# Performance work log

Measured on AMD Instinct MI355X. Metric: run time of the kernel, lower is better.

The kernel has to match this reference:

```python
import jax, jax.numpy as jnp
import numpy as np
import math

BLOCK = 8
N_COEFF = BLOCK * BLOCK  # 64
N_SAMPLE = 250
SEED = 0  # args.seed

# zigzag order: flat index m*8+n from the hardcoded loc table
ZIGZAG = jnp.array([
    0, 1, 8, 16, 9, 2, 3, 10, 17, 24, 32, 25, 18, 11, 4, 5,
    12, 19, 26, 33, 40, 48, 41, 34, 27, 20, 13, 6, 7, 14, 21, 28,
    35, 42, 49, 56, 57, 50, 43, 36, 29, 22, 15, 23, 30, 37, 44, 51,
    58, 59, 52, 45, 38, 31, 39, 46, 53, 60, 61, 54, 47, 55, 62, 63
], dtype=jnp.int32)


def dct_matrix():
    Q = np.zeros((BLOCK, BLOCK), dtype=np.float32)
    Q[0, :] = math.sqrt(1.0 / BLOCK)
    for i in range(1, BLOCK):
        for j in range(BLOCK):
            Q[i, j] = math.sqrt(2.0 / BLOCK) * math.cos((2 * j + 1) * math.pi * i / (2.0 * BLOCK))
    return jnp.asarray(Q)


def setup_inputs() -> dict:
    key = jax.random.key(0)
    x = jax.random.uniform(key, (64, 3, 512, 512), dtype=jnp.float32)
    return {"x": x}


def reference(x):
    Q = dct_matrix()
    # rgb -> ycbcr, luminance channel only (module discards Cb/Cr)
    x255 = x * 255.0
    y = (0.299 * x255[:, 0] + 0.587 * x255[:, 1] + 0.114 * x255[:, 2]) / 255.0  # [B,H,W]
    B, H, W = y.shape
    a, b = H // BLOCK, W // BLOCK
    # split into 8x8 blocks: [B, a, b, 8, 8]
    blocks = y.reshape(B, a, BLOCK, b, BLOCK).transpose(0, 1, 3, 2, 4)
    # per-block 2D DCT: Q @ block @ Q^T, batched as one einsum
    dct = jnp.einsum('ij,nabjk,lk->nabil', Q, blocks, Q)  # [B,a,b,8,8]
    image_dct_result = dct.transpose(0, 1, 3, 2, 4).reshape(B, 1, H, W)
    # zigzag gather over flattened block coefficients -> [B, 64, a*b]
    dist = dct.reshape(B, a * b, N_COEFF)[:, :, ZIGZAG].transpose(0, 2, 1)
    # per (sample, coefficient) random permutation sampling of 250 blocks
    keys = jax.random.split(jax.random.key(SEED), B * N_COEFF)
    idx = jax.vmap(lambda k: jax.random.permutation(k, a * b)[:N_SAMPLE])(keys)
    idx = idx.reshape(B, N_COEFF, N_SAMPLE)
    dct_coeff_sample = jnp.take_along_axis(dist, idx, axis=2)  # [B,64,250]
    return image_dct_result, dct_coeff_sample
```

## Files before the change

kernel.cpp:

```cpp
#include <hip/hip_runtime.h>
#include <hip/hip_bf16.h>
#include <cstdint>


#define BATCH 64
#define HW 512
#define NBLK 4096
#define NSAMPLE 250
#define IMG_ELEMS (HW * HW)

#define A0 0.35355339059327373f
#define A1 0.49039264020161522f
#define A2 0.46193976625564337f
#define A3 0.41573480615127262f
#define A4 0.35355339059327379f
#define A5 0.27778511650980111f
#define A6 0.19134171618254492f
#define A7 0.09754516100806412f

__constant__ float Qc[8][8] = {
    { A0,  A0,  A0,  A0,  A0,  A0,  A0,  A0},
    { A1,  A3,  A5,  A7, -A7, -A5, -A3, -A1},
    { A2,  A6, -A6, -A2, -A2, -A6,  A6,  A2},
    { A3, -A7, -A1, -A5,  A5,  A1,  A7, -A3},
    { A4, -A4, -A4,  A4,  A4, -A4, -A4,  A4},
    { A5, -A1,  A7,  A3, -A3, -A7,  A1, -A5},
    { A6, -A2,  A2, -A6, -A6,  A2, -A2,  A6},
    { A7, -A5,  A3, -A1,  A1, -A3,  A5, -A7},
};

__constant__ int ZIGZAG[64] = {
    0, 1, 8, 16, 9, 2, 3, 10, 17, 24, 32, 25, 18, 11, 4, 5,
    12, 19, 26, 33, 40, 48, 41, 34, 27, 20, 13, 6, 7, 14, 21, 28,
    35, 42, 49, 56, 57, 50, 43, 36, 29, 22, 15, 23, 30, 37, 44, 51,
    58, 59, 52, 45, 38, 31, 39, 46, 53, 60, 61, 54, 47, 55, 62, 63
};

__global__ __launch_bounds__(256) void dct_kernel(const float* __restrict__ x,
                                                  float* __restrict__ out) {
    __shared__ float ylds[8 * 8 * 32];

    const int t = threadIdx.x;
    const int wg = blockIdx.x;
    const int b = wg >> 7;
    const int ai = (wg >> 1) & 63;
    const int h = wg & 1;
    const int row0 = ai * 8;
    const int colbase = h * 256;

    {
        const int k = t >> 5;
        const int cg = t & 31;
        size_t off = (size_t)b * 3 * IMG_ELEMS + (size_t)(row0 + k) * HW +
                     colbase + cg * 8;
        float4 r0 = *(const float4*)(x + off);
        float4 r1 = *(const float4*)(x + off + 4);
        float4 g0 = *(const float4*)(x + off + IMG_ELEMS);
        float4 g1 = *(const float4*)(x + off + IMG_ELEMS + 4);
        float4 b0 = *(const float4*)(x + off + 2 * IMG_ELEMS);
        float4 b1 = *(const float4*)(x + off + 2 * IMG_ELEMS + 4);
        float R[8] = {r0.x, r0.y, r0.z, r0.w, r1.x, r1.y, r1.z, r1.w};
        float G[8] = {g0.x, g0.y, g0.z, g0.w, g1.x, g1.y, g1.z, g1.w};
        float B[8] = {b0.x, b0.y, b0.z, b0.w, b1.x, b1.y, b1.z, b1.w};
#pragma unroll
        for (int jj = 0; jj < 8; ++jj) {
            float y = (0.299f * (R[jj] * 255.0f) + 0.587f * (G[jj] * 255.0f) +
                       0.114f * (B[jj] * 255.0f)) / 255.0f;
            ylds[k * 256 + jj * 32 + cg] = y;
        }
    }
    __syncthreads();

    const int i = t >> 5;
    const int bi = t & 31;
    float qrow[8];
#pragma unroll
    for (int k = 0; k < 8; ++k) qrow[k] = Qc[i][k];

    float acc[8];
#pragma unroll
    for (int j = 0; j < 8; ++j) acc[j] = 0.0f;
#pragma unroll
    for (int k = 0; k < 8; ++k) {
#pragma unroll
        for (int j = 0; j < 8; ++j)
            acc[j] += qrow[k] * ylds[k * 256 + j * 32 + bi];
    }

    float d[8];
#pragma unroll
    for (int j = 0; j < 8; ++j) {
        float s = 0.0f;
#pragma unroll
        for (int k = 0; k < 8; ++k) s += acc[k] * Qc[j][k];
        d[j] = s;
    }
    float4* o = (float4*)(out + (size_t)b * IMG_ELEMS +
                          (size_t)(row0 + i) * HW + colbase + bi * 8);
    o[0] = make_float4(d[0], d[1], d[2], d[3]);
    o[1] = make_float4(d[4], d[5], d[6], d[7]);
}

__device__ __forceinline__ uint32_t rotl32(uint32_t v, int d) {
    return (v << d) | (v >> (32 - d));
}

__device__ __forceinline__ void tf2x32(uint32_t k0, uint32_t k1,
                                       uint32_t x0, uint32_t x1,
                                       uint32_t& o0, uint32_t& o1) {
    uint32_t ks0 = k0, ks1 = k1, ks2 = k0 ^ k1 ^ 0x1BD11BDAu;
    x0 += ks0; x1 += ks1;
#define TF_R(r) { x0 += x1; x1 = rotl32(x1, r); x1 ^= x0; }
    TF_R(13) TF_R(15) TF_R(26) TF_R(6)
    x0 += ks1; x1 += ks2 + 1u;
    TF_R(17) TF_R(29) TF_R(16) TF_R(24)
    x0 += ks2; x1 += ks0 + 2u;
    TF_R(13) TF_R(15) TF_R(26) TF_R(6)
    x0 += ks0; x1 += ks1 + 3u;
    TF_R(17) TF_R(29) TF_R(16) TF_R(24)
    x0 += ks1; x1 += ks2 + 4u;
    TF_R(13) TF_R(15) TF_R(26) TF_R(6)
    x0 += ks2; x1 += ks0 + 5u;
#undef TF_R
    o0 = x0; o1 = x1;
}

__device__ __forceinline__ void rank4096(
    uint32_t s0, uint32_t s1,
    uint32_t* __restrict__ pack32, uint32_t* __restrict__ hist32,
    uint32_t* __restrict__ slot32, bool zero_slot,
    int tid, int w, int lane, uint32_t* __restrict__ wsum,
    uint32_t ranks[8]) {
    uint16_t* hist16 = (uint16_t*)hist32;

    __syncthreads();
#pragma unroll
    for (int q = 0; q < 4; ++q) hist32[tid + q * 512] = 0u;
    if (zero_slot) {
#pragma unroll
        for (int q = 0; q < 4; ++q) slot32[tid + q * 512] = 0xFFFFFFFFu;
    }
    uint32_t keys[8];
#pragma unroll
    for (int e = 0; e < 8; ++e) {
        uint32_t o0, o1;
        tf2x32(s0, s1, 0u, (uint32_t)(tid + e * 512), o0, o1);
        keys[e] = o0 ^ o1;
    }
    __syncthreads();

    uint32_t ord[8];
#pragma unroll
    for (int e = 0; e < 8; ++e) {
        uint32_t bkt = keys[e] >> 20;
        uint32_t sh = (bkt & 1) << 4;
        uint32_t old = atomicAdd(&hist32[bkt >> 1], 1u << sh);
        ord[e] = (old >> sh) & 0xFFFFu;
    }
    __syncthreads();

    uint4 wv = ((const uint4*)hist32)[tid];
    uint32_t c0 = wv.x & 0xFFFFu, c1 = wv.x >> 16;
    uint32_t c2 = wv.y & 0xFFFFu, c3 = wv.y >> 16;
    uint32_t c4 = wv.z & 0xFFFFu, c5 = wv.z >> 16;
    uint32_t c6 = wv.w & 0xFFFFu, c7 = wv.w >> 16;
    uint32_t ssum = c0 + c1 + c2 + c3 + c4 + c5 + c6 + c7;
    uint32_t sc = ssum;
#pragma unroll
    for (int off = 1; off < 64; off <<= 1) {
        uint32_t t = __shfl_up(sc, off);
        if (lane >= off) sc += t;
    }
    if (lane == 63) wsum[w] = sc;
    __syncthreads();
    uint32_t ex = sc - ssum;
    for (int ww = 0; ww < w; ++ww) ex += wsum[ww];
    uint32_t p1 = ex + c0, p2 = p1 + c1, p3 = p2 + c2, p4 = p3 + c3;
    uint32_t p5 = p4 + c4, p6 = p5 + c5, p7 = p6 + c6, p8 = p7 + c7;
    uint4 ov;
    ov.x = p1 | (p2 << 16); ov.y = p3 | (p4 << 16);
    ov.z = p5 | (p6 << 16); ov.w = p7 | (p8 << 16);
    ((uint4*)hist32)[tid] = ov;
    __syncthreads();

#pragma unroll
    for (int e = 0; e < 8; ++e) {
        uint32_t bkt = keys[e] >> 20;
        uint32_t start = bkt ? (uint32_t)hist16[bkt - 1] : 0u;
        pack32[start + ord[e]] =
            ((keys[e] & 0xFFFFFu) << 12) | (uint32_t)(tid + e * 512);
        ord[e] = start;
    }
    __syncthreads();

#pragma unroll
    for (int e = 0; e < 8; ++e) {
        uint32_t bkt = keys[e] >> 20;
        uint32_t start = ord[e];
        uint32_t end = (uint32_t)hist16[bkt];
        uint32_t self = ((keys[e] & 0xFFFFFu) << 12) | (uint32_t)(tid + e * 512);
        uint32_t r = start;
        for (uint32_t p = start; p < end; ++p)
            r += (pack32[p] < self) ? 1u : 0u;
        ranks[e] = r;
    }
}

__global__ __launch_bounds__(512) void sample_kernel(const float* __restrict__ img,
                                                     float* __restrict__ out2) {
    __shared__ __align__(16) uint32_t pack32[NBLK];
    __shared__ __align__(16) uint32_t hist32[2048];
    __shared__ __align__(16) uint32_t slot32[2048];
    __shared__ uint32_t wsum[8];
    uint16_t* slot16 = (uint16_t*)slot32;

    const int tid = threadIdx.x;
    const int w = tid >> 6;
    const int lane = tid & 63;
    const int gb = blockIdx.x;

    uint32_t k0, k1, n0, n1, sA0, sA1, sB0, sB1;
    tf2x32(0u, 0u, 0u, (uint32_t)gb, k0, k1);
    tf2x32(k0, k1, 0u, 0u, n0, n1);
    tf2x32(k0, k1, 0u, 1u, sA0, sA1);
    tf2x32(n0, n1, 0u, 1u, sB0, sB1);

    uint32_t ranks[8];

    rank4096(sB0, sB1, pack32, hist32, slot32, true, tid, w, lane, wsum, ranks);
#pragma unroll
    for (int e = 0; e < 8; ++e)
        if (ranks[e] < NSAMPLE) slot16[tid + e * 512] = (uint16_t)ranks[e];

    rank4096(sA0, sA1, pack32, hist32, slot32, false, tid, w, lane, wsum, ranks);

    int b = gb >> 6, c = gb & 63;
    int z = ZIGZAG[c];
    int i0z = z >> 3, j0z = z & 7;
    const float* base = img + (size_t)b * IMG_ELEMS;
#pragma unroll
    for (int e = 0; e < 8; ++e) {
        uint32_t s = slot16[ranks[e]];
        if (s != 0xFFFFu) {
            int i = tid + e * 512;
            int ai = i >> 6, bi = i & 63;
            out2[(size_t)gb * NSAMPLE + s] =
                base[(size_t)(ai * 8 + i0z) * HW + (bi * 8 + j0z)];
        }
    }
}

extern "C" void kernel_launch(void* const* d_in, const int* in_sizes, int n_in,
                              void* d_out, int out_size, void* d_ws, size_t ws_size,
                              hipStream_t stream) {
    const float* x = (const float*)d_in[0];
    float* out = (float*)d_out;
    dct_kernel<<<BATCH * 128, 256, 0, stream>>>(x, out);
    sample_kernel<<<BATCH * 64, 512, 0, stream>>>(out, out + (size_t)BATCH * IMG_ELEMS);
}
```

Measured before the change: 414.4 us.

## Replace full rank computation with binary-search selection of only needed samples

Instead of computing the sorted rank of all 4096 keys in both permutation rounds and scattering through a slot table, each permutation's bucket histogram and packed keys are built, then only the 250 needed positions are resolved by binary search over the prefix histogram plus an in-bucket selection. The first round selects 250 indices, the second maps them through the second permutation. This removes the per-element in-bucket rank loops and the slot table, leaving 250 threads doing the selection work while the rest idle. In-bucket selection is quadratic in bucket size, which is small for random keys.

```diff
diff --git a/kernel.cpp b/kernel.cpp
--- a/kernel.cpp
+++ b/kernel.cpp
@@ -125,21 +125,15 @@
     o0 = x0; o1 = x1;
 }
 
-__device__ __forceinline__ void rank4096(
+__device__ __forceinline__ void build4096(
     uint32_t s0, uint32_t s1,
     uint32_t* __restrict__ pack32, uint32_t* __restrict__ hist32,
-    uint32_t* __restrict__ slot32, bool zero_slot,
-    int tid, int w, int lane, uint32_t* __restrict__ wsum,
-    uint32_t ranks[8]) {
+    int tid, int w, int lane, uint32_t* __restrict__ wsum) {
     uint16_t* hist16 = (uint16_t*)hist32;
 
     __syncthreads();
 #pragma unroll
     for (int q = 0; q < 4; ++q) hist32[tid + q * 512] = 0u;
-    if (zero_slot) {
-#pragma unroll
-        for (int q = 0; q < 4; ++q) slot32[tid + q * 512] = 0xFFFFFFFFu;
-    }
     uint32_t keys[8];
 #pragma unroll
     for (int e = 0; e < 8; ++e) {
@@ -189,30 +183,42 @@
         uint32_t start = bkt ? (uint32_t)hist16[bkt - 1] : 0u;
         pack32[start + ord[e]] =
             ((keys[e] & 0xFFFFFu) << 12) | (uint32_t)(tid + e * 512);
-        ord[e] = start;
-    }
-    __syncthreads();
-
-#pragma unroll
-    for (int e = 0; e < 8; ++e) {
-        uint32_t bkt = keys[e] >> 20;
-        uint32_t start = ord[e];
-        uint32_t end = (uint32_t)hist16[bkt];
-        uint32_t self = ((keys[e] & 0xFFFFFu) << 12) | (uint32_t)(tid + e * 512);
-        uint32_t r = start;
-        for (uint32_t p = start; p < end; ++p)
-            r += (pack32[p] < self) ? 1u : 0u;
-        ranks[e] = r;
-    }
+    }
+}
+
+__device__ __forceinline__ uint32_t select4096(
+    const uint16_t* __restrict__ hist16, const uint32_t* __restrict__ pack32,
+    uint32_t s) {
+    uint32_t lo = 0, hi = 4095;
+#pragma unroll
+    for (int it = 0; it < 12; ++it) {
+        uint32_t mid = (lo + hi) >> 1;
+        if ((uint32_t)hist16[mid] > s) hi = mid; else lo = mid + 1;
+    }
+    uint32_t b = lo;
+    uint32_t start = b ? (uint32_t)hist16[b - 1] : 0u;
+    uint32_t L = (uint32_t)hist16[b] - start;
+    uint32_t c = pack32[start];
+    if (L > 1) {
+        uint32_t k = s - start;
+        for (uint32_t cand = 0; cand < L; ++cand) {
+            uint32_t cc = pack32[start + cand];
+            uint32_t cnt = 0;
+            for (uint32_t o = 0; o < L; ++o)
+                cnt += (pack32[start + o] < cc) ? 1u : 0u;
+            if (cnt == k) { c = cc; break; }
+        }
+    }
+    return c & 0xFFFu;
 }
 
 __global__ __launch_bounds__(512) void sample_kernel(const float* __restrict__ img,
                                                      float* __restrict__ out2) {
     __shared__ __align__(16) uint32_t pack32[NBLK];
     __shared__ __align__(16) uint32_t hist32[2048];
-    __shared__ __align__(16) uint32_t slot32[2048];
+    __shared__ uint16_t jsel[256];
     __shared__ uint32_t wsum[8];
-    uint16_t* slot16 = (uint16_t*)slot32;
+    uint16_t* hist16 = (uint16_t*)hist32;
 
     const int tid = threadIdx.x;
     const int w = tid >> 6;
@@ -225,28 +231,23 @@
     tf2x32(k0, k1, 0u, 1u, sA0, sA1);
     tf2x32(n0, n1, 0u, 1u, sB0, sB1);
 
-    uint32_t ranks[8];
-
-    rank4096(sB0, sB1, pack32, hist32, slot32, true, tid, w, lane, wsum, ranks);
-#pragma unroll
-    for (int e = 0; e < 8; ++e)
-        if (ranks[e] < NSAMPLE) slot16[tid + e * 512] = (uint16_t)ranks[e];
-
-    rank4096(sA0, sA1, pack32, hist32, slot32, false, tid, w, lane, wsum, ranks);
+    build4096(sB0, sB1, pack32, hist32, tid, w, lane, wsum);
+    __syncthreads();
+    if (tid < NSAMPLE)
+        jsel[tid] = (uint16_t)select4096(hist16, pack32, (uint32_t)tid);
+
+    build4096(sA0, sA1, pack32, hist32, tid, w, lane, wsum);
+    __syncthreads();
 
     int b = gb >> 6, c = gb & 63;
     int z = ZIGZAG[c];
     int i0z = z >> 3, j0z = z & 7;
-    const float* base = img + (size_t)b * IMG_ELEMS;
-#pragma unroll
-    for (int e = 0; e < 8; ++e) {
-        uint32_t s = slot16[ranks[e]];
-        if (s != 0xFFFFu) {
-            int i = tid + e * 512;
-            int ai = i >> 6, bi = i & 63;
-            out2[(size_t)gb * NSAMPLE + s] =
-                base[(size_t)(ai * 8 + i0z) * HW + (bi * 8 + j0z)];
-        }
+    if (tid < NSAMPLE) {
+        uint32_t i = select4096(hist16, pack32, (uint32_t)jsel[tid]);
+        int ai = (int)i >> 6, bi = (int)i & 63;
+        out2[(size_t)gb * NSAMPLE + tid] =
+            img[(size_t)b * IMG_ELEMS + (size_t)(ai * 8 + i0z) * HW +
+                (bi * 8 + j0z)];
     }
 }
 
```

Result: faster. 392.0 us (-5.4%).
